# Kernel tuning notes

Hardware: AMD Instinct MI355X
Metric: run time of the kernel (lower is better)

The kernel has to match this reference:

```python
import jax, jax.numpy as jnp
import numpy as np

N_NODES = 50000
N_EDGES = 800000
N_GRAPHS = 512
H = 64
F_NODE = 32
F_EDGE = 8
N_CLASSES = 10
EPS = 1e-5


def _bn(x, w, b):
    # BatchNorm1d in training mode: batch stats, biased variance
    m = jnp.mean(x, axis=0)
    v = jnp.mean(jnp.square(x - m), axis=0)
    return (x - m) * jax.lax.rsqrt(v + EPS) * w + b


def setup_inputs() -> dict:
    key = jax.random.key(0)
    ks = jax.random.split(key, 12)
    s = 0.02
    inp = {
        "x": jax.random.normal(ks[0], (N_NODES, F_NODE), jnp.float32),
        "edge_attr": jax.random.normal(ks[1], (N_EDGES, F_EDGE), jnp.float32),
        "edge_index": jax.random.randint(ks[2], (2, N_EDGES), 0, N_NODES),
        "batch": jnp.sort(jax.random.randint(ks[3], (N_NODES,), 0, N_GRAPHS)),
        "bn_feat_w": jnp.ones((F_NODE,), jnp.float32),
        "bn_feat_b": jnp.full((F_NODE,), 1e-4, jnp.float32),
        "Wn0": jax.random.normal(ks[4], (F_NODE, H), jnp.float32) * s,
        "bn0": jnp.zeros((H,), jnp.float32),
        "We0": jax.random.normal(ks[5], (2 * H + F_EDGE, H), jnp.float32) * s,
        "be0": jnp.zeros((H,), jnp.float32),
        "bns_w": jnp.ones((3, H), jnp.float32),
        "bns_b": jnp.full((3, H), 1e-4, jnp.float32),
        "Wn": jax.random.normal(ks[6], (3, H, H), jnp.float32) * s,
        "Wnb": jnp.zeros((3, H), jnp.float32),
        "We": jax.random.normal(ks[7], (3, 3 * H, H), jnp.float32) * s,
        "Web": jnp.zeros((3, H), jnp.float32),
        "bn_fc_w": jnp.ones((H,), jnp.float32),
        "bn_fc_b": jnp.full((H,), 1e-4, jnp.float32),
        "Wfc": jax.random.normal(ks[8], (H, H), jnp.float32) * s,
        "bfc": jnp.zeros((H,), jnp.float32),
        "bn_hid_w": jnp.ones((H,), jnp.float32),
        "bn_hid_b": jnp.full((H,), 1e-4, jnp.float32),
        "Wcls": jax.random.normal(ks[9], (H, N_CLASSES), jnp.float32) * s,
        "bcls": jnp.zeros((N_CLASSES,), jnp.float32),
    }
    return inp


def reference(x, edge_attr, edge_index, batch, bn_feat_w, bn_feat_b, Wn0, bn0,
              We0, be0, bns_w, bns_b, Wn, Wnb, We, Web, bn_fc_w, bn_fc_b,
              Wfc, bfc, bn_hid_w, bn_hid_b, Wcls, bcls):
    src, dst = edge_index[0], edge_index[1]
    n = x.shape[0]
    # symmetric GCN edge normalization (edge_norm=True)
    deg = jax.ops.segment_sum(jnp.ones_like(src, jnp.float32), dst, num_segments=n)
    dinv = jax.lax.rsqrt(jnp.maximum(deg, 1.0))
    norm = (dinv[src] * dinv[dst])[:, None]  # [E,1]

    # feature conv (gfn=True: linear transforms only, no propagation)
    h = _bn(x, bn_feat_w, bn_feat_b) @ Wn0 + bn0  # [N,H]
    e = (h[src] @ We0[:H] + h[dst] @ We0[H:2 * H]
         + edge_attr @ We0[2 * H:] + be0)         # [E,H]
    h = jax.nn.relu(h)
    e = jax.nn.relu(e)

    # stacked edge-gated GCN convs: BN -> conv(gather/scatter) -> ReLU
    for i in range(3):
        ht = _bn(h, bns_w[i], bns_b[i]) @ Wn[i] + Wnb[i]          # [N,H]
        hs = ht[src]                                               # [E,H] gather
        ei = (hs @ We[i, :H] + ht[dst] @ We[i, H:2 * H]
              + e @ We[i, 2 * H:] + Web[i])                        # [E,H]
        msg = norm * hs * jax.nn.sigmoid(ei)                       # edge-gated message
        h = jax.nn.relu(jax.ops.segment_sum(msg, dst, num_segments=n))

    # global_add_pool over graphs
    g = jax.ops.segment_sum(h, batch, num_segments=N_GRAPHS)       # [G,H]
    g = jax.nn.relu(_bn(g, bn_fc_w, bn_fc_b) @ Wfc + bfc)
    g = _bn(g, bn_hid_w, bn_hid_b) @ Wcls + bcls
    return jax.nn.log_softmax(g, axis=-1)
```

## Files before the change

kernel.cpp:

```cpp
#include <hip/hip_runtime.h>
#include <hip/hip_bf16.h>

#define N_NODESC 50000
#define N_EDGESC 800000
#define N_GRAPHSC 512
#define HDIM 64
#define FNODE 32
#define FEDGE 8
#define NCLS 10
#define BN_EPS 1e-5f
#define SCAN_B 256
#define SCAN_G 196
#define NPW 4

typedef __bf16 bf16x8 __attribute__((ext_vector_type(8)));
typedef float f32x4 __attribute__((ext_vector_type(4)));
typedef unsigned int uint32;

static __device__ __forceinline__ float bcast(float v, int k) {
  return __uint_as_float(__builtin_amdgcn_readlane(__float_as_uint(v), k));
}
static __device__ __forceinline__ unsigned short f2bu(float f) {
  __hip_bfloat16 b = __float2bfloat16(f);
  return *reinterpret_cast<unsigned short*>(&b);
}
static __device__ __forceinline__ float bu2f(unsigned short u) {
  __hip_bfloat16 b;
  *reinterpret_cast<unsigned short*>(&b) = u;
  return __bfloat162float(b);
}

__global__ void k_deg(const int* __restrict__ dst, uint32* __restrict__ degi) {
  int e = blockIdx.x * blockDim.x + threadIdx.x;
  if (e < N_EDGESC) atomicAdd(&degi[dst[e]], 1u);
}

__global__ void k_dinv(const uint32* __restrict__ degi, float* __restrict__ dinv) {
  int n = blockIdx.x * blockDim.x + threadIdx.x;
  if (n < N_NODESC) dinv[n] = rsqrtf(fmaxf((float)degi[n], 1.0f));
}

__global__ void k_scan1(const uint32* __restrict__ degi, uint32* __restrict__ ptr,
                        uint32* __restrict__ bsum) {
  __shared__ uint32 s[SCAN_B];
  int t = threadIdx.x;
  int i = blockIdx.x * SCAN_B + t;
  uint32 v = (i < N_NODESC) ? degi[i] : 0u;
  s[t] = v; __syncthreads();
  for (int off = 1; off < SCAN_B; off <<= 1) {
    uint32 x = (t >= off) ? s[t - off] : 0u; __syncthreads();
    s[t] += x; __syncthreads();
  }
  if (i < N_NODESC) ptr[i] = s[t] - v;
  if (t == SCAN_B - 1) bsum[blockIdx.x] = s[t];
}

__global__ void k_scan2(uint32* __restrict__ bsum) {
  __shared__ uint32 s[256];
  int t = threadIdx.x;
  uint32 v = (t < SCAN_G) ? bsum[t] : 0u;
  s[t] = v; __syncthreads();
  for (int off = 1; off < 256; off <<= 1) {
    uint32 x = (t >= off) ? s[t - off] : 0u; __syncthreads();
    s[t] += x; __syncthreads();
  }
  if (t < SCAN_G) bsum[t] = s[t] - v;
}

__global__ void k_scan3(uint32* __restrict__ ptr, const uint32* __restrict__ bsum) {
  int i = blockIdx.x * SCAN_B + threadIdx.x;
  if (i < N_NODESC) ptr[i] += bsum[blockIdx.x];
  if (blockIdx.x == 0 && threadIdx.x == 0) ptr[N_NODESC] = N_EDGESC;
}

__global__ void k_scatter(const int* __restrict__ src, const int* __restrict__ dst,
                          const float* __restrict__ ea, const float* __restrict__ dinv,
                          const uint32* __restrict__ ptr, uint32* __restrict__ cursor,
                          int* __restrict__ srcs, int* __restrict__ dsts,
                          float* __restrict__ ea_s, float* __restrict__ normf) {
  int e = blockIdx.x * blockDim.x + threadIdx.x;
  if (e < N_EDGESC) {
    int d = dst[e];
    int s = src[e];
    float4 a0 = *reinterpret_cast<const float4*>(ea + (size_t)e * FEDGE);
    float4 a1 = *reinterpret_cast<const float4*>(ea + (size_t)e * FEDGE + 4);
    uint32 r = atomicAdd(&cursor[d], 1u);
    uint32 i = ptr[d] + r;
    srcs[i] = s;
    dsts[i] = d;
    normf[i] = dinv[s] * dinv[d];
    *reinterpret_cast<float4*>(ea_s + (size_t)i * FEDGE) = a0;
    *reinterpret_cast<float4*>(ea_s + (size_t)i * FEDGE + 4) = a1;
  }
}

template <int C>
__global__ void k_colstats(const float* __restrict__ in, int nrows, float* __restrict__ stats) {
  const int RPB = 256 / C;
  int tid = threadIdx.x;
  int col = tid % C;
  int rowOff = tid / C;
  float s = 0.f, s2 = 0.f;
  for (int r = blockIdx.x * RPB + rowOff; r < nrows; r += gridDim.x * RPB) {
    float v = in[r * C + col];
    s += v; s2 += v * v;
  }
  __shared__ float ls[256], ls2[256];
  ls[tid] = s; ls2[tid] = s2;
  __syncthreads();
  for (int off = 128; off >= C; off >>= 1) {
    if (tid < off) { ls[tid] += ls[tid + off]; ls2[tid] += ls2[tid + off]; }
    __syncthreads();
  }
  if (tid < C) {
    atomicAdd(&stats[tid], ls[tid]);
    atomicAdd(&stats[C + tid], ls2[tid]);
  }
}

template <int CIN, int COUT>
__global__ void k_foldbn(const float* __restrict__ stats, float invN,
                         const float* __restrict__ bnw, const float* __restrict__ bnb,
                         const float* __restrict__ W, const float* __restrict__ bias,
                         float* __restrict__ Wf, float* __restrict__ bf) {
  __shared__ float a[CIN], sh[CIN];
  int tid = threadIdx.x;
  if (tid < CIN) {
    float m = stats[tid] * invN;
    float v = stats[CIN + tid] * invN - m * m;
    float inv = rsqrtf(v + BN_EPS);
    float aa = bnw[tid] * inv;
    a[tid] = aa;
    sh[tid] = bnb[tid] - m * aa;
  }
  __syncthreads();
  for (int i = tid; i < CIN * COUT; i += 256) {
    int r = i / COUT;
    Wf[i] = a[r] * W[i];
  }
  if (tid < COUT) {
    float acc = bias ? bias[tid] : 0.f;
    for (int r = 0; r < CIN; ++r) acc += sh[r] * W[r * COUT + tid];
    bf[tid] = acc;
  }
}

template <int K, bool RELU>
__global__ void k_nodemm(const float* __restrict__ in, int nrows,
                         const float* __restrict__ W, const float* __restrict__ bias,
                         float* __restrict__ out) {
  int tid = threadIdx.x;
  int lane = tid & 63;
  float w[K];
#pragma unroll
  for (int k = 0; k < K; ++k) w[k] = W[k * 64 + lane];
  float bv = bias ? bias[lane] : 0.f;
  int wave = (blockIdx.x * blockDim.x + tid) >> 6;
  int nwaves = (gridDim.x * blockDim.x) >> 6;
  for (int r = wave; r < nrows; r += nwaves) {
    float rv = (lane < K) ? in[(size_t)r * K + lane] : 0.f;
    float acc = bv;
#pragma unroll
    for (int k = 0; k < K; ++k) acc = fmaf(bcast(rv, k), w[k], acc);
    if (RELU) acc = fmaxf(acc, 0.f);
    out[(size_t)r * 64 + lane] = acc;
  }
}

__global__ void __launch_bounds__(256, 2) k_stage0(
    const float* __restrict__ x, int nrows,
    const float* __restrict__ Wf, const float* __restrict__ bfv,
    const float* __restrict__ WA, const float* __restrict__ bA,
    const float* __restrict__ WB,
    float* __restrict__ h, unsigned short* __restrict__ hAb,
    unsigned short* __restrict__ hBb) {
  int tid = threadIdx.x;
  int lane = tid & 63;
  float w0[FNODE], wA[64], wB[64];
#pragma unroll
  for (int k = 0; k < FNODE; ++k) w0[k] = Wf[k * 64 + lane];
#pragma unroll
  for (int k = 0; k < 64; ++k) wA[k] = WA[k * 64 + lane];
#pragma unroll
  for (int k = 0; k < 64; ++k) wB[k] = WB[k * 64 + lane];
  float b0 = bfv[lane];
  float b2 = bA[lane];
  int wave = (blockIdx.x * blockDim.x + tid) >> 6;
  int nwaves = (gridDim.x * blockDim.x) >> 6;
  for (int r = wave; r < nrows; r += nwaves) {
    float xv = (lane < FNODE) ? x[(size_t)r * FNODE + lane] : 0.f;
    float t0 = b0;
#pragma unroll
    for (int k = 0; k < FNODE; ++k) t0 = fmaf(bcast(xv, k), w0[k], t0);
    float aA = b2, aB = 0.f;
#pragma unroll
    for (int k = 0; k < 64; ++k) {
      float tb = bcast(t0, k);
      aA = fmaf(tb, wA[k], aA);
      aB = fmaf(tb, wB[k], aB);
    }
    h[(size_t)r * 64 + lane] = fmaxf(t0, 0.f);
    hAb[(size_t)r * 64 + lane] = f2bu(aA);
    hBb[(size_t)r * 64 + lane] = f2bu(aB);
  }
}

__global__ void __launch_bounds__(256, 2) k_node3(
    const float* __restrict__ h, int nrows,
    const float* __restrict__ stats, float invN,
    const float* __restrict__ bnw, const float* __restrict__ bnb,
    const float* __restrict__ Wn_i, const float* __restrict__ Wnb_i,
    const float* __restrict__ WA, const float* __restrict__ Wab,
    const float* __restrict__ WB,
    uint32* __restrict__ htP, unsigned short* __restrict__ htBb) {
  __shared__ float a_s[64], sh_s[64];
  int tid = threadIdx.x;
  int lane = tid & 63;
  if (tid < 64) {
    float m = stats[tid] * invN;
    float v = stats[64 + tid] * invN - m * m;
    float inv = rsqrtf(v + BN_EPS);
    float aa = bnw[tid] * inv;
    a_s[tid] = aa;
    sh_s[tid] = bnb[tid] - m * aa;
  }
  __syncthreads();
  float w1[64], w2[64], w3[64];
  float b1 = Wnb_i[lane];
#pragma unroll
  for (int k = 0; k < 64; ++k) {
    float raw = Wn_i[k * 64 + lane];
    w1[k] = a_s[k] * raw;
    b1 = fmaf(sh_s[k], raw, b1);
  }
#pragma unroll
  for (int k = 0; k < 64; ++k) w2[k] = WA[k * 64 + lane];
#pragma unroll
  for (int k = 0; k < 64; ++k) w3[k] = WB[k * 64 + lane];
  float b2 = Wab[lane];
  int cperm = (lane & 15) * 4 + (lane >> 4);
  int wave = (blockIdx.x * blockDim.x + tid) >> 6;
  int nwaves = (gridDim.x * blockDim.x) >> 6;
  for (int r = wave; r < nrows; r += nwaves) {
    float hv = h[(size_t)r * 64 + lane];
    float t1 = b1;
#pragma unroll
    for (int k = 0; k < 64; ++k) t1 = fmaf(bcast(hv, k), w1[k], t1);
    float t2 = b2;
    float t3 = 0.f;
#pragma unroll
    for (int k = 0; k < 64; ++k) {
      float tb = bcast(t1, k);
      t2 = fmaf(tb, w2[k], t2);
      t3 = fmaf(tb, w3[k], t3);
    }
    htP[(size_t)r * 64 + cperm] = ((uint32)f2bu(t2) << 16) | (uint32)f2bu(t1);
    htBb[(size_t)r * 64 + lane] = f2bu(t3);
  }
}

__global__ void k_edgeinit(const unsigned short* __restrict__ hAb,
                           const unsigned short* __restrict__ hBb,
                           const float* __restrict__ ea_s, const float* __restrict__ Wc,
                           const int* __restrict__ srcs, const int* __restrict__ dsts,
                           __hip_bfloat16* __restrict__ ebf) {
  int tid = threadIdx.x;
  int lane = tid & 63;
  float w[FEDGE];
#pragma unroll
  for (int k = 0; k < FEDGE; ++k) w[k] = Wc[k * 64 + lane];
  int wave = (blockIdx.x * blockDim.x + tid) >> 6;
  int nwaves = (gridDim.x * blockDim.x) >> 6;
  const int nquads = N_EDGESC / 4;
  int per = (nquads + nwaves - 1) / nwaves;
  int p0 = wave * per;
  int p1 = min(p0 + per, nquads);
  if (p0 >= p1) return;
  bool el = (lane < FEDGE);
  int e = 4 * p0;
  int s0 = srcs[e], s1 = srcs[e + 1], s2 = srcs[e + 2], s3 = srcs[e + 3];
  int d0 = dsts[e], d1 = dsts[e + 1], d2 = dsts[e + 2], d3 = dsts[e + 3];
  for (int pr = p0; pr < p1; ++pr) {
    e = 4 * pr;
    unsigned short a0 = hAb[s0 * 64 + lane], b0 = hBb[d0 * 64 + lane];
    unsigned short a1 = hAb[s1 * 64 + lane], b1 = hBb[d1 * 64 + lane];
    unsigned short a2 = hAb[s2 * 64 + lane], b2 = hBb[d2 * 64 + lane];
    unsigned short a3 = hAb[s3 * 64 + lane], b3 = hBb[d3 * 64 + lane];
    float av0 = el ? ea_s[(size_t)e * FEDGE + lane] : 0.f;
    float av1 = el ? ea_s[(size_t)(e + 1) * FEDGE + lane] : 0.f;
    float av2 = el ? ea_s[(size_t)(e + 2) * FEDGE + lane] : 0.f;
    float av3 = el ? ea_s[(size_t)(e + 3) * FEDGE + lane] : 0.f;
    if (pr + 1 < p1) {
      int en = 4 * (pr + 1);
      s0 = srcs[en]; s1 = srcs[en + 1]; s2 = srcs[en + 2]; s3 = srcs[en + 3];
      d0 = dsts[en]; d1 = dsts[en + 1]; d2 = dsts[en + 2]; d3 = dsts[en + 3];
    }
    float acc0 = bu2f(a0) + bu2f(b0);
    float acc1 = bu2f(a1) + bu2f(b1);
    float acc2 = bu2f(a2) + bu2f(b2);
    float acc3 = bu2f(a3) + bu2f(b3);
#pragma unroll
    for (int k = 0; k < FEDGE; ++k) {
      acc0 = fmaf(bcast(av0, k), w[k], acc0);
      acc1 = fmaf(bcast(av1, k), w[k], acc1);
      acc2 = fmaf(bcast(av2, k), w[k], acc2);
      acc3 = fmaf(bcast(av3, k), w[k], acc3);
    }
    unsigned short* ob = reinterpret_cast<unsigned short*>(ebf);
    __builtin_nontemporal_store(f2bu(fmaxf(acc0, 0.f)), ob + (size_t)e * 64 + lane);
    __builtin_nontemporal_store(f2bu(fmaxf(acc1, 0.f)), ob + (size_t)(e + 1) * 64 + lane);
    __builtin_nontemporal_store(f2bu(fmaxf(acc2, 0.f)), ob + (size_t)(e + 2) * 64 + lane);
    __builtin_nontemporal_store(f2bu(fmaxf(acc3, 0.f)), ob + (size_t)(e + 3) * 64 + lane);
  }
}

__global__ void __launch_bounds__(256, 4) k_conv_mfma(
    const __hip_bfloat16* __restrict__ ebf,
    const float* __restrict__ We2,
    const uint32* __restrict__ htP, const unsigned short* __restrict__ htBb,
    const float* __restrict__ normf,
    const int* __restrict__ srcs, const int* __restrict__ dsts,
    const uint32* __restrict__ ptr,
    float* __restrict__ hout, float* __restrict__ stats) {
  __shared__ float lds_acc[4][NPW * 65];
  __shared__ float lds_htB[4][NPW * 65];
  __shared__ float st_s[64], st_s2[64];
  const int tid = threadIdx.x;
  const int lane = tid & 63;
  const int w = tid >> 6;
  const int m = lane & 15;
  const int kg = lane >> 4;

  int wave = blockIdx.x * 4 + w;
  int n0 = wave * NPW;

  if (stats && tid < 64) { st_s[tid] = 0.f; st_s2[tid] = 0.f; }
  if (stats) __syncthreads();

  bf16x8 b[4][2];
#pragma unroll
  for (int t = 0; t < 4; ++t)
#pragma unroll
    for (int s = 0; s < 2; ++s)
#pragma unroll
      for (int j = 0; j < 8; ++j) {
        int k = s * 32 + kg * 8 + j;
        int c = t * 16 + m;
        b[t][s][j] = (__bf16)We2[k * 64 + c];
      }

  float* acc_l = lds_acc[w];
  float* htB_l = lds_htB[w];
#pragma unroll
  for (int r = 0; r < NPW; ++r) {
    acc_l[r * 65 + lane] = 0.f;
    htB_l[r * 65 + lane] = bu2f(htBb[(size_t)(n0 + r) * 64 + lane]);
  }

  int e0 = (int)ptr[n0];
  int eend = (int)ptr[n0 + NPW];
  int tb0 = e0 & ~15;

  float run[4] = {0.f, 0.f, 0.f, 0.f};
  int dcur = -1, rcur = 0;

  for (int tb = tb0; tb < eend; tb += 16) {
    const bf16x8* arow = reinterpret_cast<const bf16x8*>(ebf + (size_t)(tb + m) * 64 + kg * 8);
    bf16x8 a0 = __builtin_nontemporal_load(arow);
    bf16x8 a1 = __builtin_nontemporal_load(arow + 4);
    int rb = tb + kg * 4;
    int4 sev = *reinterpret_cast<const int4*>(srcs + rb);
    int4 dev = *reinterpret_cast<const int4*>(dsts + rb);
    float4 nev = *reinterpret_cast<const float4*>(normf + rb);
    int se[4] = {sev.x, sev.y, sev.z, sev.w};
    int de[4] = {dev.x, dev.y, dev.z, dev.w};
    float ne[4] = {nev.x, nev.y, nev.z, nev.w};
    uint4 pv[4];
#pragma unroll
    for (int j = 0; j < 4; ++j)
      pv[j] = *reinterpret_cast<const uint4*>(htP + (size_t)se[j] * 64 + m * 4);

    f32x4 acc[4];
#pragma unroll
    for (int t = 0; t < 4; ++t) {
      f32x4 z = {0.f, 0.f, 0.f, 0.f};
      acc[t] = __builtin_amdgcn_mfma_f32_16x16x32_bf16(a0, b[t][0], z, 0, 0, 0);
      acc[t] = __builtin_amdgcn_mfma_f32_16x16x32_bf16(a1, b[t][1], acc[t], 0, 0, 0);
    }

#pragma unroll
    for (int j = 0; j < 4; ++j) {
      int eidx = rb + j;
      bool valid = (eidx >= e0) && (eidx < eend);
      if (valid) {
        if (de[j] != dcur) {
          if (dcur >= 0) {
#pragma unroll
            for (int t = 0; t < 4; ++t) {
              atomicAdd(&acc_l[rcur * 65 + t * 16 + m], run[t]);
              run[t] = 0.f;
            }
          }
          dcur = de[j];
          rcur = dcur - n0;
        }
        uint32 pd[4] = {pv[j].x, pv[j].y, pv[j].z, pv[j].w};
#pragma unroll
        for (int t = 0; t < 4; ++t) {
          int c = t * 16 + m;
          float gate = acc[t][j] + bu2f((unsigned short)(pd[t] >> 16)) + htB_l[rcur * 65 + c];
          float sig = 1.0f / (1.0f + __expf(-gate));
          run[t] = fmaf(ne[j] * bu2f((unsigned short)(pd[t] & 0xffffu)), sig, run[t]);
        }
      }
    }
  }
  if (dcur >= 0) {
#pragma unroll
    for (int t = 0; t < 4; ++t)
      atomicAdd(&acc_l[rcur * 65 + t * 16 + m], run[t]);
  }
  float s = 0.f, s2 = 0.f;
#pragma unroll
  for (int r = 0; r < NPW; ++r) {
    float v = fmaxf(acc_l[r * 65 + lane], 0.f);
    hout[(size_t)(n0 + r) * 64 + lane] = v;
    s += v; s2 += v * v;
  }
  if (stats) {
    atomicAdd(&st_s[lane], s);
    atomicAdd(&st_s2[lane], s2);
    __syncthreads();
    if (tid < 64) atomicAdd(&stats[tid], st_s[tid]);
    else if (tid < 128) atomicAdd(&stats[tid], st_s2[tid - 64]);
  }
}

__global__ void k_pool(const float* __restrict__ h, const int* __restrict__ batch,
                       float* __restrict__ g) {
  int lane = threadIdx.x & 63;
  int wave = (blockIdx.x * blockDim.x + threadIdx.x) >> 6;
  int nwaves = (gridDim.x * blockDim.x) >> 6;
  int chunk = (N_NODESC + nwaves - 1) / nwaves;
  int r0 = wave * chunk;
  int r1 = min(r0 + chunk, N_NODESC);
  if (r0 >= r1) return;
  int cur = batch[r0];
  float acc = 0.f;
  for (int r = r0; r < r1; ++r) {
    int b = batch[r];
    if (b != cur) {
      atomicAdd(&g[cur * 64 + lane], acc);
      acc = 0.f;
      cur = b;
    }
    acc += h[r * 64 + lane];
  }
  atomicAdd(&g[cur * 64 + lane], acc);
}

__global__ void k_cls(const float* __restrict__ g2, const float* __restrict__ Wc,
                      const float* __restrict__ bc, float* __restrict__ out) {
  int r = blockIdx.x * blockDim.x + threadIdx.x;
  if (r >= N_GRAPHSC) return;
  float z[NCLS];
#pragma unroll
  for (int c = 0; c < NCLS; ++c) z[c] = bc[c];
  for (int k = 0; k < HDIM; ++k) {
    float v = g2[r * HDIM + k];
#pragma unroll
    for (int c = 0; c < NCLS; ++c) z[c] = fmaf(v, Wc[k * NCLS + c], z[c]);
  }
  float m = z[0];
#pragma unroll
  for (int c = 1; c < NCLS; ++c) m = fmaxf(m, z[c]);
  float ssum = 0.f;
#pragma unroll
  for (int c = 0; c < NCLS; ++c) ssum += __expf(z[c] - m);
  float l = __logf(ssum);
#pragma unroll
  for (int c = 0; c < NCLS; ++c) out[r * NCLS + c] = z[c] - m - l;
}

extern "C" void kernel_launch(void* const* d_in, const int* in_sizes, int n_in,
                              void* d_out, int out_size, void* d_ws, size_t ws_size,
                              hipStream_t stream) {
  const float* x         = (const float*)d_in[0];
  const float* edge_attr = (const float*)d_in[1];
  const int*   ei        = (const int*)d_in[2];
  const int*   batch     = (const int*)d_in[3];
  const float* bn_feat_w = (const float*)d_in[4];
  const float* bn_feat_b = (const float*)d_in[5];
  const float* Wn0       = (const float*)d_in[6];
  const float* bn0       = (const float*)d_in[7];
  const float* We0       = (const float*)d_in[8];
  const float* be0       = (const float*)d_in[9];
  const float* bns_w     = (const float*)d_in[10];
  const float* bns_b     = (const float*)d_in[11];
  const float* Wn        = (const float*)d_in[12];
  const float* Wnb       = (const float*)d_in[13];
  const float* We        = (const float*)d_in[14];
  const float* Web       = (const float*)d_in[15];
  const float* bn_fc_w   = (const float*)d_in[16];
  const float* bn_fc_b   = (const float*)d_in[17];
  const float* Wfc       = (const float*)d_in[18];
  const float* bfc       = (const float*)d_in[19];
  const float* bn_hid_w  = (const float*)d_in[20];
  const float* bn_hid_b  = (const float*)d_in[21];
  const float* Wcls      = (const float*)d_in[22];
  const float* bcls      = (const float*)d_in[23];
  float* out = (float*)d_out;
  const int* src = ei;
  const int* dst = ei + N_EDGESC;

  char* p = (char*)d_ws;
  auto carve = [&](size_t bytes) {
    char* q = p;
    p += (bytes + 255) & ~(size_t)255;
    return q;
  };
  __hip_bfloat16* ebf = (__hip_bfloat16*)carve((size_t)N_EDGESC * 64 * 2);
  float* h    = (float*)carve((size_t)N_NODESC * 64 * 4);
  uint32* htP = (uint32*)carve((size_t)N_NODESC * 64 * 4);
  unsigned short* htBb = (unsigned short*)carve((size_t)N_NODESC * 64 * 2);
  unsigned short* hAb  = (unsigned short*)carve((size_t)N_NODESC * 64 * 2);
  unsigned short* hBb  = (unsigned short*)carve((size_t)N_NODESC * 64 * 2);
  float* dinv = (float*)carve((size_t)N_NODESC * 4);
  float* g    = (float*)carve((size_t)N_GRAPHSC * 64 * 4);
  float* g2   = (float*)carve((size_t)N_GRAPHSC * 64 * 4);
  float* stats= (float*)carve(6 * 128 * 4);
  float* Wf   = (float*)carve(64 * 64 * 4);
  float* bf   = (float*)carve(64 * 4);
  uint32* degi   = (uint32*)carve((size_t)50176 * 4);
  uint32* ptr    = (uint32*)carve((size_t)50176 * 4);
  uint32* cursor = (uint32*)carve((size_t)50176 * 4);
  uint32* bsum   = (uint32*)carve(256 * 4);
  int* srcs  = (int*)carve((size_t)N_EDGESC * 4);
  int* dsts  = (int*)carve((size_t)N_EDGESC * 4);
  float* ea_s  = (float*)carve((size_t)N_EDGESC * FEDGE * 4);
  float* normf = (float*)carve((size_t)N_EDGESC * 4);

  float* st_x  = stats;
  float* st_h0 = stats + 128;
  float* st_h1 = stats + 256;
  float* st_h2 = stats + 384;
  float* st_g  = stats + 512;
  float* st_g2 = stats + 640;

  hipMemsetAsync(degi, 0, (size_t)3 * 50176 * 4, stream);
  hipMemsetAsync(stats, 0, 6 * 128 * 4, stream);

  k_deg<<<(N_EDGESC + 255) / 256, 256, 0, stream>>>(dst, degi);
  k_dinv<<<(N_NODESC + 255) / 256, 256, 0, stream>>>(degi, dinv);
  k_scan1<<<SCAN_G, SCAN_B, 0, stream>>>(degi, ptr, bsum);
  k_scan2<<<1, 256, 0, stream>>>(bsum);
  k_scan3<<<SCAN_G, SCAN_B, 0, stream>>>(ptr, bsum);
  k_scatter<<<(N_EDGESC + 255) / 256, 256, 0, stream>>>(src, dst, edge_attr, dinv, ptr, cursor,
                                                        srcs, dsts, ea_s, normf);

  k_colstats<FNODE><<<256, 256, 0, stream>>>(x, N_NODESC, st_x);
  k_foldbn<FNODE, HDIM><<<1, 256, 0, stream>>>(st_x, 1.f / N_NODESC, bn_feat_w, bn_feat_b, Wn0, bn0, Wf, bf);
  k_stage0<<<512, 256, 0, stream>>>(x, N_NODESC, Wf, bf, We0, be0, We0 + 64 * 64, h, hAb, hBb);
  k_edgeinit<<<1024, 256, 0, stream>>>(hAb, hBb, ea_s, We0 + 128 * 64, srcs, dsts, ebf);
  k_colstats<HDIM><<<256, 256, 0, stream>>>(h, N_NODESC, st_h0);

  const int convBlocks = N_NODESC / (NPW * 4);
  float* inSlot[3]  = {st_h0, st_h1, st_h2};
  float* outSlot[3] = {st_h1, st_h2, nullptr};
  for (int i = 0; i < 3; ++i) {
    const float* WeI = We + (size_t)i * 192 * 64;
    k_node3<<<512, 256, 0, stream>>>(h, N_NODESC, inSlot[i], 1.f / N_NODESC,
                                     bns_w + i * 64, bns_b + i * 64,
                                     Wn + (size_t)i * 64 * 64, Wnb + i * 64,
                                     WeI, Web + i * 64, WeI + 64 * 64, htP, htBb);
    k_conv_mfma<<<convBlocks, 256, 0, stream>>>(ebf, WeI + 128 * 64, htP, htBb, normf,
                                                srcs, dsts, ptr, h, outSlot[i]);
  }

  hipMemsetAsync(g, 0, N_GRAPHSC * 64 * 4, stream);
  k_pool<<<64, 256, 0, stream>>>(h, batch, g);
  k_colstats<HDIM><<<32, 256, 0, stream>>>(g, N_GRAPHSC, st_g);
  k_foldbn<HDIM, HDIM><<<1, 256, 0, stream>>>(st_g, 1.f / N_GRAPHSC, bn_fc_w, bn_fc_b, Wfc, bfc, Wf, bf);
  k_nodemm<HDIM, true><<<128, 256, 0, stream>>>(g, N_GRAPHSC, Wf, bf, g2);
  k_colstats<HDIM><<<32, 256, 0, stream>>>(g2, N_GRAPHSC, st_g2);
  k_foldbn<HDIM, NCLS><<<1, 256, 0, stream>>>(st_g2, 1.f / N_GRAPHSC, bn_hid_w, bn_hid_b, Wcls, bcls, Wf, bf);
  k_cls<<<(N_GRAPHSC + 255) / 256, 256, 0, stream>>>(g2, Wf, bf, out);
}
```

Measured before the change: 782.7 us.

## Fuse CSR scatter into edge init, pool into last conv, dinv into scan

Merges the edge scatter pass into the edge-init kernel, so edges are processed in input order, scattered to their CSR slot by atomics, and the bf16 edge embedding is written directly to the sorted position. The sorted edge-attribute buffer and its write and read-back go away. Global add pooling is fused into the last conv's epilogue, which skips writing h, and dinv is computed inside scan1. Nodes per wave in the conv kernel doubles to 8, with bounds guards for the partial tail. The trade-off is scattered writes for the edge embeddings, lane-0..3 atomics inside a wave loop, and fewer conv waves.

```diff
diff --git a/kernel.cpp b/kernel.cpp
--- a/kernel.cpp
+++ b/kernel.cpp
@@ -11,7 +11,7 @@
 #define BN_EPS 1e-5f
 #define SCAN_B 256
 #define SCAN_G 196
-#define NPW 4
+#define NPW 8
 
 typedef __bf16 bf16x8 __attribute__((ext_vector_type(8)));
 typedef float f32x4 __attribute__((ext_vector_type(4)));
@@ -19,6 +19,9 @@
 
 static __device__ __forceinline__ float bcast(float v, int k) {
   return __uint_as_float(__builtin_amdgcn_readlane(__float_as_uint(v), k));
+}
+static __device__ __forceinline__ int bcast_i(int v, int k) {
+  return __builtin_amdgcn_readlane(v, k);
 }
 static __device__ __forceinline__ unsigned short f2bu(float f) {
   __hip_bfloat16 b = __float2bfloat16(f);
@@ -35,17 +38,13 @@
   if (e < N_EDGESC) atomicAdd(&degi[dst[e]], 1u);
 }
 
-__global__ void k_dinv(const uint32* __restrict__ degi, float* __restrict__ dinv) {
-  int n = blockIdx.x * blockDim.x + threadIdx.x;
-  if (n < N_NODESC) dinv[n] = rsqrtf(fmaxf((float)degi[n], 1.0f));
-}
-
 __global__ void k_scan1(const uint32* __restrict__ degi, uint32* __restrict__ ptr,
-                        uint32* __restrict__ bsum) {
+                        uint32* __restrict__ bsum, float* __restrict__ dinv) {
   __shared__ uint32 s[SCAN_B];
   int t = threadIdx.x;
   int i = blockIdx.x * SCAN_B + t;
   uint32 v = (i < N_NODESC) ? degi[i] : 0u;
+  if (i < N_NODESC) dinv[i] = rsqrtf(fmaxf((float)v, 1.0f));
   s[t] = v; __syncthreads();
   for (int off = 1; off < SCAN_B; off <<= 1) {
     uint32 x = (t >= off) ? s[t - off] : 0u; __syncthreads();
@@ -71,27 +70,6 @@
   int i = blockIdx.x * SCAN_B + threadIdx.x;
   if (i < N_NODESC) ptr[i] += bsum[blockIdx.x];
   if (blockIdx.x == 0 && threadIdx.x == 0) ptr[N_NODESC] = N_EDGESC;
-}
-
-__global__ void k_scatter(const int* __restrict__ src, const int* __restrict__ dst,
-                          const float* __restrict__ ea, const float* __restrict__ dinv,
-                          const uint32* __restrict__ ptr, uint32* __restrict__ cursor,
-                          int* __restrict__ srcs, int* __restrict__ dsts,
-                          float* __restrict__ ea_s, float* __restrict__ normf) {
-  int e = blockIdx.x * blockDim.x + threadIdx.x;
-  if (e < N_EDGESC) {
-    int d = dst[e];
-    int s = src[e];
-    float4 a0 = *reinterpret_cast<const float4*>(ea + (size_t)e * FEDGE);
-    float4 a1 = *reinterpret_cast<const float4*>(ea + (size_t)e * FEDGE + 4);
-    uint32 r = atomicAdd(&cursor[d], 1u);
-    uint32 i = ptr[d] + r;
-    srcs[i] = s;
-    dsts[i] = d;
-    normf[i] = dinv[s] * dinv[d];
-    *reinterpret_cast<float4*>(ea_s + (size_t)i * FEDGE) = a0;
-    *reinterpret_cast<float4*>(ea_s + (size_t)i * FEDGE + 4) = a1;
-  }
 }
 
 template <int C>
@@ -259,11 +237,14 @@
   }
 }
 
-__global__ void k_edgeinit(const unsigned short* __restrict__ hAb,
-                           const unsigned short* __restrict__ hBb,
-                           const float* __restrict__ ea_s, const float* __restrict__ Wc,
-                           const int* __restrict__ srcs, const int* __restrict__ dsts,
-                           __hip_bfloat16* __restrict__ ebf) {
+__global__ void k_scatedge(
+    const int* __restrict__ src, const int* __restrict__ dst,
+    const float* __restrict__ ea, const float* __restrict__ dinv,
+    const uint32* __restrict__ ptr, uint32* __restrict__ cursor,
+    const unsigned short* __restrict__ hAb, const unsigned short* __restrict__ hBb,
+    const float* __restrict__ Wc,
+    int* __restrict__ srcs, int* __restrict__ dsts, float* __restrict__ normf,
+    __hip_bfloat16* __restrict__ ebf) {
   int tid = threadIdx.x;
   int lane = tid & 63;
   float w[FEDGE];
@@ -275,42 +256,45 @@
   int per = (nquads + nwaves - 1) / nwaves;
   int p0 = wave * per;
   int p1 = min(p0 + per, nquads);
-  if (p0 >= p1) return;
-  bool el = (lane < FEDGE);
-  int e = 4 * p0;
-  int s0 = srcs[e], s1 = srcs[e + 1], s2 = srcs[e + 2], s3 = srcs[e + 3];
-  int d0 = dsts[e], d1 = dsts[e + 1], d2 = dsts[e + 2], d3 = dsts[e + 3];
   for (int pr = p0; pr < p1; ++pr) {
-    e = 4 * pr;
-    unsigned short a0 = hAb[s0 * 64 + lane], b0 = hBb[d0 * 64 + lane];
-    unsigned short a1 = hAb[s1 * 64 + lane], b1 = hBb[d1 * 64 + lane];
-    unsigned short a2 = hAb[s2 * 64 + lane], b2 = hBb[d2 * 64 + lane];
-    unsigned short a3 = hAb[s3 * 64 + lane], b3 = hBb[d3 * 64 + lane];
-    float av0 = el ? ea_s[(size_t)e * FEDGE + lane] : 0.f;
-    float av1 = el ? ea_s[(size_t)(e + 1) * FEDGE + lane] : 0.f;
-    float av2 = el ? ea_s[(size_t)(e + 2) * FEDGE + lane] : 0.f;
-    float av3 = el ? ea_s[(size_t)(e + 3) * FEDGE + lane] : 0.f;
-    if (pr + 1 < p1) {
-      int en = 4 * (pr + 1);
-      s0 = srcs[en]; s1 = srcs[en + 1]; s2 = srcs[en + 2]; s3 = srcs[en + 3];
-      d0 = dsts[en]; d1 = dsts[en + 1]; d2 = dsts[en + 2]; d3 = dsts[en + 3];
-    }
+    int e = 4 * pr;
+    int sv = (lane < 4) ? src[e + lane] : 0;
+    int dv = (lane < 4) ? dst[e + lane] : 0;
+    int s_j[4], d_j[4];
+#pragma unroll
+    for (int j = 0; j < 4; ++j) { s_j[j] = bcast_i(sv, j); d_j[j] = bcast_i(dv, j); }
+    uint32 idx_l = 0;
+    if (lane < 4) {
+      uint32 rk = atomicAdd(&cursor[dv], 1u);
+      idx_l = ptr[dv] + rk;
+      srcs[idx_l] = sv;
+      dsts[idx_l] = dv;
+      normf[idx_l] = dinv[sv] * dinv[dv];
+    }
+    int i_j[4];
+#pragma unroll
+    for (int j = 0; j < 4; ++j) i_j[j] = bcast_i((int)idx_l, j);
+    float eav = (lane < 32) ? ea[(size_t)e * FEDGE + lane] : 0.f;
+    unsigned short a0 = hAb[(size_t)s_j[0] * 64 + lane], b0 = hBb[(size_t)d_j[0] * 64 + lane];
+    unsigned short a1 = hAb[(size_t)s_j[1] * 64 + lane], b1 = hBb[(size_t)d_j[1] * 64 + lane];
+    unsigned short a2 = hAb[(size_t)s_j[2] * 64 + lane], b2 = hBb[(size_t)d_j[2] * 64 + lane];
+    unsigned short a3 = hAb[(size_t)s_j[3] * 64 + lane], b3 = hBb[(size_t)d_j[3] * 64 + lane];
     float acc0 = bu2f(a0) + bu2f(b0);
     float acc1 = bu2f(a1) + bu2f(b1);
     float acc2 = bu2f(a2) + bu2f(b2);
     float acc3 = bu2f(a3) + bu2f(b3);
 #pragma unroll
     for (int k = 0; k < FEDGE; ++k) {
-      acc0 = fmaf(bcast(av0, k), w[k], acc0);
-      acc1 = fmaf(bcast(av1, k), w[k], acc1);
-      acc2 = fmaf(bcast(av2, k), w[k], acc2);
-      acc3 = fmaf(bcast(av3, k), w[k], acc3);
+      acc0 = fmaf(bcast(eav, 0 * 8 + k), w[k], acc0);
+      acc1 = fmaf(bcast(eav, 1 * 8 + k), w[k], acc1);
+      acc2 = fmaf(bcast(eav, 2 * 8 + k), w[k], acc2);
+      acc3 = fmaf(bcast(eav, 3 * 8 + k), w[k], acc3);
     }
     unsigned short* ob = reinterpret_cast<unsigned short*>(ebf);
-    __builtin_nontemporal_store(f2bu(fmaxf(acc0, 0.f)), ob + (size_t)e * 64 + lane);
-    __builtin_nontemporal_store(f2bu(fmaxf(acc1, 0.f)), ob + (size_t)(e + 1) * 64 + lane);
-    __builtin_nontemporal_store(f2bu(fmaxf(acc2, 0.f)), ob + (size_t)(e + 2) * 64 + lane);
-    __builtin_nontemporal_store(f2bu(fmaxf(acc3, 0.f)), ob + (size_t)(e + 3) * 64 + lane);
+    __builtin_nontemporal_store(f2bu(fmaxf(acc0, 0.f)), ob + (size_t)i_j[0] * 64 + lane);
+    __builtin_nontemporal_store(f2bu(fmaxf(acc1, 0.f)), ob + (size_t)i_j[1] * 64 + lane);
+    __builtin_nontemporal_store(f2bu(fmaxf(acc2, 0.f)), ob + (size_t)i_j[2] * 64 + lane);
+    __builtin_nontemporal_store(f2bu(fmaxf(acc3, 0.f)), ob + (size_t)i_j[3] * 64 + lane);
   }
 }
 
@@ -321,7 +305,8 @@
     const float* __restrict__ normf,
     const int* __restrict__ srcs, const int* __restrict__ dsts,
     const uint32* __restrict__ ptr,
-    float* __restrict__ hout, float* __restrict__ stats) {
+    float* __restrict__ hout, float* __restrict__ stats,
+    const int* __restrict__ batch, float* __restrict__ gout) {
   __shared__ float lds_acc[4][NPW * 65];
   __shared__ float lds_htB[4][NPW * 65];
   __shared__ float st_s[64], st_s2[64];
@@ -333,9 +318,12 @@
 
   int wave = blockIdx.x * 4 + w;
   int n0 = wave * NPW;
-
-  if (stats && tid < 64) { st_s[tid] = 0.f; st_s2[tid] = 0.f; }
-  if (stats) __syncthreads();
+  bool validw = (n0 < N_NODESC);
+
+  if (stats) {
+    if (tid < 64) { st_s[tid] = 0.f; st_s2[tid] = 0.f; }
+    __syncthreads();
+  }
 
   bf16x8 b[4][2];
 #pragma unroll
@@ -354,11 +342,11 @@
 #pragma unroll
   for (int r = 0; r < NPW; ++r) {
     acc_l[r * 65 + lane] = 0.f;
-    htB_l[r * 65 + lane] = bu2f(htBb[(size_t)(n0 + r) * 64 + lane]);
-  }
-
-  int e0 = (int)ptr[n0];
-  int eend = (int)ptr[n0 + NPW];
+    htB_l[r * 65 + lane] = validw ? bu2f(htBb[(size_t)(n0 + r) * 64 + lane]) : 0.f;
+  }
+
+  int e0 = validw ? (int)ptr[n0] : 0;
+  int eend = validw ? (int)ptr[n0 + NPW] : 0;
   int tb0 = e0 & ~15;
 
   float run[4] = {0.f, 0.f, 0.f, 0.f};
@@ -420,43 +408,42 @@
     for (int t = 0; t < 4; ++t)
       atomicAdd(&acc_l[rcur * 65 + t * 16 + m], run[t]);
   }
-  float s = 0.f, s2 = 0.f;
-#pragma unroll
-  for (int r = 0; r < NPW; ++r) {
-    float v = fmaxf(acc_l[r * 65 + lane], 0.f);
-    hout[(size_t)(n0 + r) * 64 + lane] = v;
-    s += v; s2 += v * v;
-  }
-  if (stats) {
-    atomicAdd(&st_s[lane], s);
-    atomicAdd(&st_s2[lane], s2);
-    __syncthreads();
-    if (tid < 64) atomicAdd(&stats[tid], st_s[tid]);
-    else if (tid < 128) atomicAdd(&stats[tid], st_s2[tid - 64]);
-  }
-}
-
-__global__ void k_pool(const float* __restrict__ h, const int* __restrict__ batch,
-                       float* __restrict__ g) {
-  int lane = threadIdx.x & 63;
-  int wave = (blockIdx.x * blockDim.x + threadIdx.x) >> 6;
-  int nwaves = (gridDim.x * blockDim.x) >> 6;
-  int chunk = (N_NODESC + nwaves - 1) / nwaves;
-  int r0 = wave * chunk;
-  int r1 = min(r0 + chunk, N_NODESC);
-  if (r0 >= r1) return;
-  int cur = batch[r0];
-  float acc = 0.f;
-  for (int r = r0; r < r1; ++r) {
-    int b = batch[r];
-    if (b != cur) {
-      atomicAdd(&g[cur * 64 + lane], acc);
-      acc = 0.f;
-      cur = b;
-    }
-    acc += h[r * 64 + lane];
-  }
-  atomicAdd(&g[cur * 64 + lane], acc);
+
+  if (gout) {
+    if (validw) {
+      int bcur = batch[n0];
+      float racc = 0.f;
+#pragma unroll
+      for (int r = 0; r < NPW; ++r) {
+        float v = fmaxf(acc_l[r * 65 + lane], 0.f);
+        int bb = batch[n0 + r];
+        if (bb != bcur) {
+          atomicAdd(&gout[(size_t)bcur * 64 + lane], racc);
+          racc = 0.f;
+          bcur = bb;
+        }
+        racc += v;
+      }
+      atomicAdd(&gout[(size_t)bcur * 64 + lane], racc);
+    }
+  } else {
+    float s = 0.f, s2 = 0.f;
+    if (validw) {
+#pragma unroll
+      for (int r = 0; r < NPW; ++r) {
+        float v = fmaxf(acc_l[r * 65 + lane], 0.f);
+        hout[(size_t)(n0 + r) * 64 + lane] = v;
+        s += v; s2 += v * v;
+      }
+    }
+    if (stats) {
+      atomicAdd(&st_s[lane], s);
+      atomicAdd(&st_s2[lane], s2);
+      __syncthreads();
+      if (tid < 64) atomicAdd(&stats[tid], st_s[tid]);
+      else if (tid < 128) atomicAdd(&stats[tid], st_s2[tid - 64]);
+    }
+  }
 }
 
 __global__ void k_cls(const float* __restrict__ g2, const float* __restrict__ Wc,
@@ -537,7 +524,6 @@
   uint32* bsum   = (uint32*)carve(256 * 4);
   int* srcs  = (int*)carve((size_t)N_EDGESC * 4);
   int* dsts  = (int*)carve((size_t)N_EDGESC * 4);
-  float* ea_s  = (float*)carve((size_t)N_EDGESC * FEDGE * 4);
   float* normf = (float*)carve((size_t)N_EDGESC * 4);
 
   float* st_x  = stats;
@@ -549,22 +535,22 @@
 
   hipMemsetAsync(degi, 0, (size_t)3 * 50176 * 4, stream);
   hipMemsetAsync(stats, 0, 6 * 128 * 4, stream);
+  hipMemsetAsync(g, 0, N_GRAPHSC * 64 * 4, stream);
 
   k_deg<<<(N_EDGESC + 255) / 256, 256, 0, stream>>>(dst, degi);
-  k_dinv<<<(N_NODESC + 255) / 256, 256, 0, stream>>>(degi, dinv);
-  k_scan1<<<SCAN_G, SCAN_B, 0, stream>>>(degi, ptr, bsum);
+  k_scan1<<<SCAN_G, SCAN_B, 0, stream>>>(degi, ptr, bsum, dinv);
   k_scan2<<<1, 256, 0, stream>>>(bsum);
   k_scan3<<<SCAN_G, SCAN_B, 0, stream>>>(ptr, bsum);
-  k_scatter<<<(N_EDGESC + 255) / 256, 256, 0, stream>>>(src, dst, edge_attr, dinv, ptr, cursor,
-                                                        srcs, dsts, ea_s, normf);
 
   k_colstats<FNODE><<<256, 256, 0, stream>>>(x, N_NODESC, st_x);
   k_foldbn<FNODE, HDIM><<<1, 256, 0, stream>>>(st_x, 1.f / N_NODESC, bn_feat_w, bn_feat_b, Wn0, bn0, Wf, bf);
   k_stage0<<<512, 256, 0, stream>>>(x, N_NODESC, Wf, bf, We0, be0, We0 + 64 * 64, h, hAb, hBb);
-  k_edgeinit<<<1024, 256, 0, stream>>>(hAb, hBb, ea_s, We0 + 128 * 64, srcs, dsts, ebf);
+
+  k_scatedge<<<1024, 256, 0, stream>>>(src, dst, edge_attr, dinv, ptr, cursor,
+                                       hAb, hBb, We0 + 128 * 64, srcs, dsts, normf, ebf);
   k_colstats<HDIM><<<256, 256, 0, stream>>>(h, N_NODESC, st_h0);
 
-  const int convBlocks = N_NODESC / (NPW * 4);
+  const int convBlocks = (N_NODESC / NPW + 3) / 4;
   float* inSlot[3]  = {st_h0, st_h1, st_h2};
   float* outSlot[3] = {st_h1, st_h2, nullptr};
   for (int i = 0; i < 3; ++i) {
@@ -574,11 +560,10 @@
                                      Wn + (size_t)i * 64 * 64, Wnb + i * 64,
                                      WeI, Web + i * 64, WeI + 64 * 64, htP, htBb);
     k_conv_mfma<<<convBlocks, 256, 0, stream>>>(ebf, WeI + 128 * 64, htP, htBb, normf,
-                                                srcs, dsts, ptr, h, outSlot[i]);
-  }
-
-  hipMemsetAsync(g, 0, N_GRAPHSC * 64 * 4, stream);
-  k_pool<<<64, 256, 0, stream>>>(h, batch, g);
+                                                srcs, dsts, ptr, h, outSlot[i],
+                                                batch, (i == 2) ? g : nullptr);
+  }
+
   k_colstats<HDIM><<<32, 256, 0, stream>>>(g, N_GRAPHSC, st_g);
   k_foldbn<HDIM, HDIM><<<1, 256, 0, stream>>>(st_g, 1.f / N_GRAPHSC, bn_fc_w, bn_fc_b, Wfc, bfc, Wf, bf);
   k_nodemm<HDIM, true><<<128, 256, 0, stream>>>(g, N_GRAPHSC, Wf, bf, g2);
```

Result: faster. 679.8 us (-13.2%).

## Fuse global add pooling into final conv and dinv into scan

Applied to the files above, without the earlier changes.

The final edge-gated conv now adds its ReLU outputs straight into the per-graph pooled buffer, using the sorted batch ids, so the separate pooling kernel and the write of the last h are gone. The dinv computation moves into the first scan kernel, which removes one launch. Nodes per wave go from 4 to 8 and the grid rounds up with a validity guard, which halves the number of waves and changes load balance and LDS use per block.

```diff
diff --git a/kernel.cpp b/kernel.cpp
--- a/kernel.cpp
+++ b/kernel.cpp
@@ -11,7 +11,7 @@
 #define BN_EPS 1e-5f
 #define SCAN_B 256
 #define SCAN_G 196
-#define NPW 4
+#define NPW 8
 
 typedef __bf16 bf16x8 __attribute__((ext_vector_type(8)));
 typedef float f32x4 __attribute__((ext_vector_type(4)));
@@ -35,17 +35,13 @@
   if (e < N_EDGESC) atomicAdd(&degi[dst[e]], 1u);
 }
 
-__global__ void k_dinv(const uint32* __restrict__ degi, float* __restrict__ dinv) {
-  int n = blockIdx.x * blockDim.x + threadIdx.x;
-  if (n < N_NODESC) dinv[n] = rsqrtf(fmaxf((float)degi[n], 1.0f));
-}
-
 __global__ void k_scan1(const uint32* __restrict__ degi, uint32* __restrict__ ptr,
-                        uint32* __restrict__ bsum) {
+                        uint32* __restrict__ bsum, float* __restrict__ dinv) {
   __shared__ uint32 s[SCAN_B];
   int t = threadIdx.x;
   int i = blockIdx.x * SCAN_B + t;
   uint32 v = (i < N_NODESC) ? degi[i] : 0u;
+  if (i < N_NODESC) dinv[i] = rsqrtf(fmaxf((float)v, 1.0f));
   s[t] = v; __syncthreads();
   for (int off = 1; off < SCAN_B; off <<= 1) {
     uint32 x = (t >= off) ? s[t - off] : 0u; __syncthreads();
@@ -321,7 +317,8 @@
     const float* __restrict__ normf,
     const int* __restrict__ srcs, const int* __restrict__ dsts,
     const uint32* __restrict__ ptr,
-    float* __restrict__ hout, float* __restrict__ stats) {
+    float* __restrict__ hout, float* __restrict__ stats,
+    const int* __restrict__ batch, float* __restrict__ gout) {
   __shared__ float lds_acc[4][NPW * 65];
   __shared__ float lds_htB[4][NPW * 65];
   __shared__ float st_s[64], st_s2[64];
@@ -333,9 +330,12 @@
 
   int wave = blockIdx.x * 4 + w;
   int n0 = wave * NPW;
-
-  if (stats && tid < 64) { st_s[tid] = 0.f; st_s2[tid] = 0.f; }
-  if (stats) __syncthreads();
+  bool validw = (n0 < N_NODESC);
+
+  if (stats) {
+    if (tid < 64) { st_s[tid] = 0.f; st_s2[tid] = 0.f; }
+    __syncthreads();
+  }
 
   bf16x8 b[4][2];
 #pragma unroll
@@ -354,11 +354,11 @@
 #pragma unroll
   for (int r = 0; r < NPW; ++r) {
     acc_l[r * 65 + lane] = 0.f;
-    htB_l[r * 65 + lane] = bu2f(htBb[(size_t)(n0 + r) * 64 + lane]);
-  }
-
-  int e0 = (int)ptr[n0];
-  int eend = (int)ptr[n0 + NPW];
+    htB_l[r * 65 + lane] = validw ? bu2f(htBb[(size_t)(n0 + r) * 64 + lane]) : 0.f;
+  }
+
+  int e0 = validw ? (int)ptr[n0] : 0;
+  int eend = validw ? (int)ptr[n0 + NPW] : 0;
   int tb0 = e0 & ~15;
 
   float run[4] = {0.f, 0.f, 0.f, 0.f};
@@ -420,43 +420,42 @@
     for (int t = 0; t < 4; ++t)
       atomicAdd(&acc_l[rcur * 65 + t * 16 + m], run[t]);
   }
-  float s = 0.f, s2 = 0.f;
-#pragma unroll
-  for (int r = 0; r < NPW; ++r) {
-    float v = fmaxf(acc_l[r * 65 + lane], 0.f);
-    hout[(size_t)(n0 + r) * 64 + lane] = v;
-    s += v; s2 += v * v;
-  }
-  if (stats) {
-    atomicAdd(&st_s[lane], s);
-    atomicAdd(&st_s2[lane], s2);
-    __syncthreads();
-    if (tid < 64) atomicAdd(&stats[tid], st_s[tid]);
-    else if (tid < 128) atomicAdd(&stats[tid], st_s2[tid - 64]);
-  }
-}
-
-__global__ void k_pool(const float* __restrict__ h, const int* __restrict__ batch,
-                       float* __restrict__ g) {
-  int lane = threadIdx.x & 63;
-  int wave = (blockIdx.x * blockDim.x + threadIdx.x) >> 6;
-  int nwaves = (gridDim.x * blockDim.x) >> 6;
-  int chunk = (N_NODESC + nwaves - 1) / nwaves;
-  int r0 = wave * chunk;
-  int r1 = min(r0 + chunk, N_NODESC);
-  if (r0 >= r1) return;
-  int cur = batch[r0];
-  float acc = 0.f;
-  for (int r = r0; r < r1; ++r) {
-    int b = batch[r];
-    if (b != cur) {
-      atomicAdd(&g[cur * 64 + lane], acc);
-      acc = 0.f;
-      cur = b;
-    }
-    acc += h[r * 64 + lane];
-  }
-  atomicAdd(&g[cur * 64 + lane], acc);
+
+  if (gout) {
+    if (validw) {
+      int bcur = batch[n0];
+      float racc = 0.f;
+#pragma unroll
+      for (int r = 0; r < NPW; ++r) {
+        float v = fmaxf(acc_l[r * 65 + lane], 0.f);
+        int bb = batch[n0 + r];
+        if (bb != bcur) {
+          atomicAdd(&gout[(size_t)bcur * 64 + lane], racc);
+          racc = 0.f;
+          bcur = bb;
+        }
+        racc += v;
+      }
+      atomicAdd(&gout[(size_t)bcur * 64 + lane], racc);
+    }
+  } else {
+    float s = 0.f, s2 = 0.f;
+    if (validw) {
+#pragma unroll
+      for (int r = 0; r < NPW; ++r) {
+        float v = fmaxf(acc_l[r * 65 + lane], 0.f);
+        hout[(size_t)(n0 + r) * 64 + lane] = v;
+        s += v; s2 += v * v;
+      }
+    }
+    if (stats) {
+      atomicAdd(&st_s[lane], s);
+      atomicAdd(&st_s2[lane], s2);
+      __syncthreads();
+      if (tid < 64) atomicAdd(&stats[tid], st_s[tid]);
+      else if (tid < 128) atomicAdd(&stats[tid], st_s2[tid - 64]);
+    }
+  }
 }
 
 __global__ void k_cls(const float* __restrict__ g2, const float* __restrict__ Wc,
@@ -549,10 +548,10 @@
 
   hipMemsetAsync(degi, 0, (size_t)3 * 50176 * 4, stream);
   hipMemsetAsync(stats, 0, 6 * 128 * 4, stream);
+  hipMemsetAsync(g, 0, N_GRAPHSC * 64 * 4, stream);
 
   k_deg<<<(N_EDGESC + 255) / 256, 256, 0, stream>>>(dst, degi);
-  k_dinv<<<(N_NODESC + 255) / 256, 256, 0, stream>>>(degi, dinv);
-  k_scan1<<<SCAN_G, SCAN_B, 0, stream>>>(degi, ptr, bsum);
+  k_scan1<<<SCAN_G, SCAN_B, 0, stream>>>(degi, ptr, bsum, dinv);
   k_scan2<<<1, 256, 0, stream>>>(bsum);
   k_scan3<<<SCAN_G, SCAN_B, 0, stream>>>(ptr, bsum);
   k_scatter<<<(N_EDGESC + 255) / 256, 256, 0, stream>>>(src, dst, edge_attr, dinv, ptr, cursor,
@@ -564,7 +563,7 @@
   k_edgeinit<<<1024, 256, 0, stream>>>(hAb, hBb, ea_s, We0 + 128 * 64, srcs, dsts, ebf);
   k_colstats<HDIM><<<256, 256, 0, stream>>>(h, N_NODESC, st_h0);
 
-  const int convBlocks = N_NODESC / (NPW * 4);
+  const int convBlocks = (N_NODESC / NPW + 3) / 4;
   float* inSlot[3]  = {st_h0, st_h1, st_h2};
   float* outSlot[3] = {st_h1, st_h2, nullptr};
   for (int i = 0; i < 3; ++i) {
@@ -574,11 +573,10 @@
                                      Wn + (size_t)i * 64 * 64, Wnb + i * 64,
                                      WeI, Web + i * 64, WeI + 64 * 64, htP, htBb);
     k_conv_mfma<<<convBlocks, 256, 0, stream>>>(ebf, WeI + 128 * 64, htP, htBb, normf,
-                                                srcs, dsts, ptr, h, outSlot[i]);
-  }
-
-  hipMemsetAsync(g, 0, N_GRAPHSC * 64 * 4, stream);
-  k_pool<<<64, 256, 0, stream>>>(h, batch, g);
+                                                srcs, dsts, ptr, h, outSlot[i],
+                                                batch, (i == 2) ? g : nullptr);
+  }
+
   k_colstats<HDIM><<<32, 256, 0, stream>>>(g, N_GRAPHSC, st_g);
   k_foldbn<HDIM, HDIM><<<1, 256, 0, stream>>>(st_g, 1.f / N_GRAPHSC, bn_fc_w, bn_fc_b, Wfc, bfc, Wf, bf);
   k_nodemm<HDIM, true><<<128, 256, 0, stream>>>(g, N_GRAPHSC, Wf, bf, g2);
```

After: 705.2 us. -9.9%, faster.
